# Performance work log

Measured on AMD Instinct MI355X. Metric: run time of the kernel, lower is better.

## Reference

```python
import jax, jax.numpy as jnp
import numpy as np

N_HEADS = 16
N_KV_HEADS = 4
N_EMBD = 1024

def setup_inputs() -> dict:
    key = jax.random.key(0)
    kx, kq, kk, kv, ko = jax.random.split(key, 5)
    B, S, E = 2, 2048, N_EMBD
    head_dim = E // N_HEADS
    kv_dim = N_KV_HEADS * head_dim  # 256
    scale = 0.02
    return {
        "x": jax.random.normal(kx, (B, S, E), dtype=jnp.float32),
        "Wq": jax.random.normal(kq, (E, E), dtype=jnp.float32) * scale,
        "Wk": jax.random.normal(kk, (E, kv_dim), dtype=jnp.float32) * scale,
        "Wv": jax.random.normal(kv, (E, kv_dim), dtype=jnp.float32) * scale,
        "Wo": jax.random.normal(ko, (E, E), dtype=jnp.float32) * scale,
    }

def reference(x, Wq, Wk, Wv, Wo):
    B, S, E = x.shape
    H, KV = N_HEADS, N_KV_HEADS
    D = E // H            # head_dim = 64
    R = H // KV           # query heads per kv head = 4
    inv_sqrt_d = 1.0 / (D ** 0.5)

    q = (x @ Wq).reshape(B, S, KV, R, D)   # group query heads by kv group
    k = (x @ Wk).reshape(B, S, KV, D)
    v = (x @ Wv).reshape(B, S, KV, D)

    # repeat_interleave(kv, R, dim=heads) == broadcast kv head g to query heads (g, r)
    scores = jnp.einsum('bqgrd,bkgd->bgrqk', q, k) * inv_sqrt_d  # [B,KV,R,S,S]
    causal = jnp.tril(jnp.ones((S, S), dtype=bool))
    scores = jnp.where(causal, scores, jnp.float32(-jnp.inf))
    attn = jax.nn.softmax(scores, axis=-1)

    out = jnp.einsum('bgrqk,bkgd->bqgrd', attn, v).reshape(B, S, E)
    return out @ Wo
```

## Files before the change

kernel.cpp:

```cpp
#include <hip/hip_runtime.h>
#include <hip/hip_bf16.h>

#define B_SZ   2
#define S_LEN  2048
#define E_DIM  1024
#define H_Q    16
#define H_KV   4
#define HD     64
#define KV_DIM 256
#define M_ROWS (B_SZ * S_LEN)
#define N_QT   (S_LEN / 64)

typedef short bf16x4 __attribute__((ext_vector_type(4)));
typedef short bf16x8 __attribute__((ext_vector_type(8)));
typedef float f32x4  __attribute__((ext_vector_type(4)));
typedef unsigned u32x2 __attribute__((ext_vector_type(2)));

#define MFMA16x32(a, b, c) __builtin_amdgcn_mfma_f32_16x16x32_bf16(a, b, c, 0, 0, 0)

#if __has_builtin(__builtin_amdgcn_mfma_f32_16x16x16bf16_1k)
#define MFMA_PV(a, b, c) __builtin_amdgcn_mfma_f32_16x16x16bf16_1k(a, b, c, 0, 0, 0)
#elif __has_builtin(__builtin_amdgcn_mfma_f32_16x16x16_bf16)
#define MFMA_PV(a, b, c) __builtin_amdgcn_mfma_f32_16x16x16_bf16(a, b, c, 0, 0, 0)
#else
static __device__ inline f32x4 mfma_pv_asm(bf16x4 a, bf16x4 b, f32x4 c) {
    asm volatile("v_mfma_f32_16x16x16_bf16 %0, %1, %2, %0"
                 : "+v"(c) : "v"(a), "v"(b));
    return c;
}
#define MFMA_PV(a, b, c) mfma_pv_asm(a, b, c)
#endif

static __device__ __forceinline__ short f32_to_bf16(float f) {
    unsigned u = __builtin_bit_cast(unsigned, f);
    u += 0x7fffu + ((u >> 16) & 1u);
    return (short)(u >> 16);
}

static __device__ __forceinline__ unsigned pack2_trunc(float a, float b) {
    unsigned ua = __builtin_bit_cast(unsigned, a);
    unsigned ub = __builtin_bit_cast(unsigned, b);
    return (ua >> 16) | (ub & 0xffff0000u);
}

static __device__ __forceinline__ void load_lds16(const short* g, short* l) {
    __builtin_amdgcn_global_load_lds(
        (const __attribute__((address_space(1))) void*)g,
        (__attribute__((address_space(3))) void*)l, 16, 0, 0);
}

__device__ __forceinline__ void transpose_body(const float* __restrict__ W,
                                               short* __restrict__ Wt,
                                               int K, int N, int bx, int by) {
    __shared__ float t[32][33];
    const int n0 = bx * 32, k0 = by * 32;
    const int tx = threadIdx.x & 31, ty = threadIdx.x >> 5;
#pragma unroll
    for (int i = 0; i < 32; i += 8)
        t[ty + i][tx] = W[(long)(k0 + ty + i) * N + n0 + tx];
    __syncthreads();
#pragma unroll
    for (int i = 0; i < 32; i += 8)
        Wt[(long)(n0 + ty + i) * K + k0 + tx] = f32_to_bf16(t[tx][ty + i]);
}

__global__ __launch_bounds__(256)
void prep(const float* __restrict__ x,
          const float* __restrict__ Wq, const float* __restrict__ Wk,
          const float* __restrict__ Wv, const float* __restrict__ Wo,
          short* __restrict__ xbf, short* __restrict__ Wqt,
          short* __restrict__ Wkt, short* __restrict__ Wvt,
          short* __restrict__ Wot) {
    const int bid = blockIdx.x;
    if (bid < 4096) {
        const int i = bid * 256 + threadIdx.x;
        float4 v = ((const float4*)x)[i];
        bf16x4 o;
        o[0] = f32_to_bf16(v.x); o[1] = f32_to_bf16(v.y);
        o[2] = f32_to_bf16(v.z); o[3] = f32_to_bf16(v.w);
        ((bf16x4*)xbf)[i] = o;
    } else if (bid < 5120) {
        const int r = bid - 4096;
        transpose_body(Wq, Wqt, E_DIM, E_DIM, r & 31, r >> 5);
    } else if (bid < 5376) {
        const int r = bid - 5120;
        transpose_body(Wk, Wkt, E_DIM, KV_DIM, r & 7, r >> 3);
    } else if (bid < 5632) {
        const int r = bid - 5376;
        transpose_body(Wv, Wvt, E_DIM, KV_DIM, r & 7, r >> 3);
    } else {
        const int r = bid - 5632;
        transpose_body(Wo, Wot, E_DIM, E_DIM, r & 31, r >> 5);
    }
}

__global__ __launch_bounds__(256)
void transpose_v(const short* __restrict__ V, short* __restrict__ Vt) {
    const int st = blockIdx.x;
    const int gb = blockIdx.y;
    const int g  = gb >> 1, b = gb & 1;
    const int s0 = st * 64;
    __shared__ short Ls[64][72];
#pragma unroll
    for (int it = 0; it < 2; ++it) {
        const int slot = threadIdx.x + it * 256;
        const int si = slot >> 3, ch = slot & 7;
        *(bf16x8*)&Ls[si][ch * 8] = *(const bf16x8*)
            &V[((long)(b * S_LEN + s0 + si)) * KV_DIM + g * HD + ch * 8];
    }
    __syncthreads();
#pragma unroll
    for (int it = 0; it < 2; ++it) {
        const int slot = threadIdx.x + it * 256;
        const int d = slot >> 3, ch = slot & 7;
        bf16x8 v;
#pragma unroll
        for (int i = 0; i < 8; ++i) v[i] = Ls[ch * 8 + i][d];
        *(bf16x8*)&Vt[((long)(gb * HD + d)) * S_LEN + s0 + ch * 8] = v;
    }
}

__device__ __forceinline__ void gemm128(const short* __restrict__ Ab,
                                        const short* __restrict__ Btb,
                                        int K, short* As, short* Bs,
                                        f32x4 acc[4][4]) {
    const int tid  = threadIdx.x;
    const int wave = tid >> 6;
    const int lane = tid & 63;
    const int lq   = lane & 15;
    const int lg   = lane >> 4;
    const int wm   = wave >> 1;
    const int wn   = wave & 1;
    const int lrow = lane >> 2;
    const int lkc  = (lane & 3) * 8;

#pragma unroll
    for (int i = 0; i < 4; ++i)
#pragma unroll
        for (int j = 0; j < 4; ++j) acc[i][j] = (f32x4){0.f, 0.f, 0.f, 0.f};

    for (int k0 = 0; k0 < K; k0 += 32) {
        __syncthreads();
#pragma unroll
        for (int it = 0; it < 2; ++it) {
            const int m0 = wave * 32 + it * 16;
            const int m  = m0 + lrow;
            load_lds16(Ab  + (size_t)m * K + k0 + lkc, As + m0 * 32);
            load_lds16(Btb + (size_t)m * K + k0 + lkc, Bs + m0 * 32);
        }
        __syncthreads();
        bf16x8 af[4], bfr[4];
#pragma unroll
        for (int i = 0; i < 4; ++i) {
            af[i]  = *(const bf16x8*)&As[(wm * 64 + i * 16 + lq) * 32 + lg * 8];
            bfr[i] = *(const bf16x8*)&Bs[(wn * 64 + i * 16 + lq) * 32 + lg * 8];
        }
#pragma unroll
        for (int i = 0; i < 4; ++i)
#pragma unroll
            for (int j = 0; j < 4; ++j)
                acc[i][j] = MFMA16x32(af[i], bfr[j], acc[i][j]);
    }
}

__global__ __launch_bounds__(256)
void qkv_gemm(const short* __restrict__ xbf,
              const short* __restrict__ Wqt, const short* __restrict__ Wkt,
              const short* __restrict__ Wvt,
              short* __restrict__ Qbf, short* __restrict__ Kbf,
              short* __restrict__ Vbf, float qscale) {
    __shared__ short As[128 * 32];
    __shared__ short Bs[128 * 32];
    const int nb = blockIdx.x;
    const int mb = blockIdx.y;
    const short* Bt; short* out; int ldc, ncol0; float alpha;
    if (nb < 8) {
        Bt = Wqt + (size_t)nb * 128 * E_DIM;
        out = Qbf; ldc = E_DIM; ncol0 = nb * 128; alpha = qscale;
    } else if (nb < 10) {
        Bt = Wkt + (size_t)(nb - 8) * 128 * E_DIM;
        out = Kbf; ldc = KV_DIM; ncol0 = (nb - 8) * 128; alpha = 1.f;
    } else {
        Bt = Wvt + (size_t)(nb - 10) * 128 * E_DIM;
        out = Vbf; ldc = KV_DIM; ncol0 = (nb - 10) * 128; alpha = 1.f;
    }
    f32x4 acc[4][4];
    gemm128(xbf + (size_t)mb * 128 * E_DIM, Bt, E_DIM, As, Bs, acc);

    const int lane = threadIdx.x & 63, wave = threadIdx.x >> 6;
    const int lq = lane & 15, lg = lane >> 4, wm = wave >> 1, wn = wave & 1;
#pragma unroll
    for (int i = 0; i < 4; ++i)
#pragma unroll
        for (int r = 0; r < 4; ++r) {
            const size_t row = (size_t)mb * 128 + wm * 64 + i * 16 + lg * 4 + r;
#pragma unroll
            for (int j = 0; j < 4; ++j)
                out[row * ldc + ncol0 + wn * 64 + j * 16 + lq] =
                    f32_to_bf16(acc[i][j][r] * alpha);
        }
}

__global__ __launch_bounds__(256)
void gemm_o(const short* __restrict__ Abf, const short* __restrict__ Wot,
            float* __restrict__ C) {
    __shared__ short As[128 * 32];
    __shared__ short Bs[128 * 32];
    const int nb = blockIdx.x;
    const int mb = blockIdx.y;
    f32x4 acc[4][4];
    gemm128(Abf + (size_t)mb * 128 * E_DIM,
            Wot + (size_t)nb * 128 * E_DIM, E_DIM, As, Bs, acc);

    const int lane = threadIdx.x & 63, wave = threadIdx.x >> 6;
    const int lq = lane & 15, lg = lane >> 4, wm = wave >> 1, wn = wave & 1;
#pragma unroll
    for (int i = 0; i < 4; ++i)
#pragma unroll
        for (int r = 0; r < 4; ++r) {
            const size_t row = (size_t)mb * 128 + wm * 64 + i * 16 + lg * 4 + r;
#pragma unroll
            for (int j = 0; j < 4; ++j)
                C[row * E_DIM + nb * 128 + wn * 64 + j * 16 + lq] =
                    acc[i][j][r];
        }
}

struct KVregs { bf16x8 k[2], v[2]; };

__device__ __forceinline__ void stage_load(const short* __restrict__ Kb,
                                           const short* __restrict__ Vtg,
                                           long b, long ks, int g,
                                           KVregs& kv) {
    const int tid = threadIdx.x;
#pragma unroll
    for (int it = 0; it < 2; ++it) {
        const int c   = tid + it * 256;
        const int row = c >> 3;
        const int ch  = c & 7;
        kv.k[it] = *(const bf16x8*)
            &Kb[(b * S_LEN + ks + row) * KV_DIM + g * HD + ch * 8];
        kv.v[it] = *(const bf16x8*)
            &Vtg[((long)(g * 2 + b) * HD + row) * S_LEN + ks + ch * 8];
    }
}

__device__ __forceinline__ void stage_write(short (*Ks)[72], short (*Vt)[72],
                                            const KVregs& kv) {
    const int tid = threadIdx.x;
#pragma unroll
    for (int it = 0; it < 2; ++it) {
        const int c   = tid + it * 256;
        const int row = c >> 3;
        const int ch  = c & 7;
        *(bf16x8*)&Ks[row][ch * 8] = kv.k[it];
        *(bf16x8*)&Vt[row][ch * 8] = kv.v[it];
    }
}

__global__ __launch_bounds__(256)
void flash_mfma(const short* __restrict__ Qb,
                const short* __restrict__ Kb,
                const short* __restrict__ Vtg,
                short* __restrict__ Ob) {
    const int pair = blockIdx.x;
    const int h    = blockIdx.y;
    const int b    = blockIdx.z;
    const int g    = h >> 2;

    const int tid  = threadIdx.x;
    const int wave = tid >> 6;
    const int lane = tid & 63;
    const int lq   = lane & 15;
    const int lg   = lane >> 4;

    __shared__ short Ks[2][64][72];
    __shared__ short Vt[2][64][72];

    for (int rep = 0; rep < 2; ++rep) {
        const int qt = rep ? (N_QT - 1 - pair) : pair;
        const int qs = qt * 64;

        const short* qrow =
            Qb + ((long)(b * S_LEN + qs + wave * 16 + lq)) * E_DIM + h * HD;
        const bf16x8 qf0 = *(const bf16x8*)(qrow + lg * 8);
        const bf16x8 qf1 = *(const bf16x8*)(qrow + 32 + lg * 8);

        f32x4 o[4];
#pragma unroll
        for (int dc = 0; dc < 4; ++dc) o[dc] = (f32x4){0.f, 0.f, 0.f, 0.f};
        float l_run = 0.f;

        KVregs kv;
        stage_load(Kb, Vtg, b, 0, g, kv);
        stage_write(Ks[0], Vt[0], kv);
        __syncthreads();

        int p = 0;
        for (int kt = 0; kt <= qt; ++kt) {
            if (kt < qt)
                stage_load(Kb, Vtg, b, (long)(kt + 1) * 64, g, kv);

            const int cmax = (kt == qt) ? wave : 3;
            f32x4 s[4];
#pragma unroll
            for (int c = 0; c < 4; ++c) {
                if (c > cmax) continue;
                bf16x8 kf0 = *(const bf16x8*)&Ks[p][c * 16 + lq][lg * 8];
                bf16x8 kf1 = *(const bf16x8*)&Ks[p][c * 16 + lq][32 + lg * 8];
                f32x4 acc = (f32x4){0.f, 0.f, 0.f, 0.f};
                acc = MFMA16x32(kf0, qf0, acc);
                acc = MFMA16x32(kf1, qf1, acc);
                s[c] = acc;
            }

            if (kt == qt) {
#pragma unroll
                for (int r = 0; r < 4; ++r)
                    if (lg * 4 + r > lq) s[wave][r] = -INFINITY;
            }

            float psum = 0.f;
#pragma unroll
            for (int c = 0; c < 4; ++c) {
                if (c > cmax) continue;
#pragma unroll
                for (int r = 0; r < 4; ++r) {
                    float pe = exp2f(s[c][r]);
                    s[c][r] = pe;
                    psum += pe;
                }
            }
            l_run += psum;

#pragma unroll
            for (int c = 0; c < 4; ++c) {
                if (c > cmax) continue;
                u32x2 packed;
                packed[0] = pack2_trunc(s[c][0], s[c][1]);
                packed[1] = pack2_trunc(s[c][2], s[c][3]);
                bf16x4 pa = __builtin_bit_cast(bf16x4, packed);
#pragma unroll
                for (int dc = 0; dc < 4; ++dc) {
                    bf16x4 vf =
                        *(const bf16x4*)&Vt[p][dc * 16 + lq][c * 16 + lg * 4];
                    o[dc] = MFMA_PV(pa, vf, o[dc]);
                }
            }

            if (kt < qt) stage_write(Ks[p ^ 1], Vt[p ^ 1], kv);
            __syncthreads();
            p ^= 1;
        }

        l_run += __shfl_xor(l_run, 16);
        l_run += __shfl_xor(l_run, 32);

#pragma unroll
        for (int r = 0; r < 4; ++r) {
            const float lT  = __shfl(l_run, lg * 4 + r);
            const float inv = 1.f / lT;
            const long base =
                ((long)(b * S_LEN + qs + wave * 16 + lg * 4 + r)) * E_DIM +
                h * HD + lq;
#pragma unroll
            for (int dc = 0; dc < 4; ++dc)
                Ob[base + dc * 16] = f32_to_bf16(o[dc][r] * inv);
        }
    }
}

extern "C" void kernel_launch(void* const* d_in, const int* in_sizes, int n_in,
                              void* d_out, int out_size, void* d_ws, size_t ws_size,
                              hipStream_t stream) {
    const float* x  = (const float*)d_in[0];
    const float* Wq = (const float*)d_in[1];
    const float* Wk = (const float*)d_in[2];
    const float* Wv = (const float*)d_in[3];
    const float* Wo = (const float*)d_in[4];
    float* out = (float*)d_out;

    short* xbf = (short*)d_ws;
    short* Wqt = xbf + (size_t)M_ROWS * E_DIM;
    short* Wkt = Wqt + (size_t)E_DIM * E_DIM;
    short* Wvt = Wkt + (size_t)KV_DIM * E_DIM;
    short* Wot = Wvt + (size_t)KV_DIM * E_DIM;
    short* Qbf = Wot + (size_t)E_DIM * E_DIM;
    short* Kbf = Qbf + (size_t)M_ROWS * E_DIM;
    short* Vbf = Kbf + (size_t)M_ROWS * KV_DIM;
    short* Abf = Vbf + (size_t)M_ROWS * KV_DIM;
    short* Vtg = Abf + (size_t)M_ROWS * E_DIM;

    const float qscale = 0.125f * 1.44269504088896340736f;

    prep<<<dim3(6656), dim3(256), 0, stream>>>(
        x, Wq, Wk, Wv, Wo, xbf, Wqt, Wkt, Wvt, Wot);
    qkv_gemm<<<dim3(12, M_ROWS / 128), dim3(256), 0, stream>>>(
        xbf, Wqt, Wkt, Wvt, Qbf, Kbf, Vbf, qscale);
    transpose_v<<<dim3(S_LEN / 64, B_SZ * H_KV), dim3(256), 0, stream>>>(
        Vbf, Vtg);
    flash_mfma<<<dim3(N_QT / 2, H_Q, B_SZ), dim3(256), 0, stream>>>(
        Qbf, Kbf, Vtg, Abf);
    gemm_o<<<dim3(E_DIM / 128, M_ROWS / 128), dim3(256), 0, stream>>>(
        Abf, Wot, out);
}
```

Baseline: 181.6 us.

## Split flash attention over KV halves with merge kernel; fuse V transpose into QKV GEMM

```diff
diff --git a/kernel.cpp b/kernel.cpp
--- a/kernel.cpp
+++ b/kernel.cpp
@@ -94,32 +94,6 @@
     }
 }
 
-__global__ __launch_bounds__(256)
-void transpose_v(const short* __restrict__ V, short* __restrict__ Vt) {
-    const int st = blockIdx.x;
-    const int gb = blockIdx.y;
-    const int g  = gb >> 1, b = gb & 1;
-    const int s0 = st * 64;
-    __shared__ short Ls[64][72];
-#pragma unroll
-    for (int it = 0; it < 2; ++it) {
-        const int slot = threadIdx.x + it * 256;
-        const int si = slot >> 3, ch = slot & 7;
-        *(bf16x8*)&Ls[si][ch * 8] = *(const bf16x8*)
-            &V[((long)(b * S_LEN + s0 + si)) * KV_DIM + g * HD + ch * 8];
-    }
-    __syncthreads();
-#pragma unroll
-    for (int it = 0; it < 2; ++it) {
-        const int slot = threadIdx.x + it * 256;
-        const int d = slot >> 3, ch = slot & 7;
-        bf16x8 v;
-#pragma unroll
-        for (int i = 0; i < 8; ++i) v[i] = Ls[ch * 8 + i][d];
-        *(bf16x8*)&Vt[((long)(gb * HD + d)) * S_LEN + s0 + ch * 8] = v;
-    }
-}
-
 __device__ __forceinline__ void gemm128(const short* __restrict__ Ab,
                                         const short* __restrict__ Btb,
                                         int K, short* As, short* Bs,
@@ -168,37 +142,54 @@
               const short* __restrict__ Wqt, const short* __restrict__ Wkt,
               const short* __restrict__ Wvt,
               short* __restrict__ Qbf, short* __restrict__ Kbf,
-              short* __restrict__ Vbf, float qscale) {
+              short* __restrict__ Vtg, float qscale) {
     __shared__ short As[128 * 32];
     __shared__ short Bs[128 * 32];
     const int nb = blockIdx.x;
     const int mb = blockIdx.y;
-    const short* Bt; short* out; int ldc, ncol0; float alpha;
-    if (nb < 8) {
-        Bt = Wqt + (size_t)nb * 128 * E_DIM;
-        out = Qbf; ldc = E_DIM; ncol0 = nb * 128; alpha = qscale;
-    } else if (nb < 10) {
-        Bt = Wkt + (size_t)(nb - 8) * 128 * E_DIM;
-        out = Kbf; ldc = KV_DIM; ncol0 = (nb - 8) * 128; alpha = 1.f;
-    } else {
-        Bt = Wvt + (size_t)(nb - 10) * 128 * E_DIM;
-        out = Vbf; ldc = KV_DIM; ncol0 = (nb - 10) * 128; alpha = 1.f;
-    }
+    const short* Bt;
+    if (nb < 8)       Bt = Wqt + (size_t)nb * 128 * E_DIM;
+    else if (nb < 10) Bt = Wkt + (size_t)(nb - 8) * 128 * E_DIM;
+    else              Bt = Wvt + (size_t)(nb - 10) * 128 * E_DIM;
+
     f32x4 acc[4][4];
     gemm128(xbf + (size_t)mb * 128 * E_DIM, Bt, E_DIM, As, Bs, acc);
 
     const int lane = threadIdx.x & 63, wave = threadIdx.x >> 6;
     const int lq = lane & 15, lg = lane >> 4, wm = wave >> 1, wn = wave & 1;
-#pragma unroll
-    for (int i = 0; i < 4; ++i)
-#pragma unroll
-        for (int r = 0; r < 4; ++r) {
-            const size_t row = (size_t)mb * 128 + wm * 64 + i * 16 + lg * 4 + r;
-#pragma unroll
-            for (int j = 0; j < 4; ++j)
-                out[row * ldc + ncol0 + wn * 64 + j * 16 + lq] =
-                    f32_to_bf16(acc[i][j][r] * alpha);
-        }
+
+    if (nb < 10) {
+        short* out; int ldc, ncol0; float alpha;
+        if (nb < 8) { out = Qbf; ldc = E_DIM; ncol0 = nb * 128; alpha = qscale; }
+        else { out = Kbf; ldc = KV_DIM; ncol0 = (nb - 8) * 128; alpha = 1.f; }
+#pragma unroll
+        for (int i = 0; i < 4; ++i)
+#pragma unroll
+            for (int r = 0; r < 4; ++r) {
+                const size_t row =
+                    (size_t)mb * 128 + wm * 64 + i * 16 + lg * 4 + r;
+#pragma unroll
+                for (int j = 0; j < 4; ++j)
+                    out[row * ldc + ncol0 + wn * 64 + j * 16 + lq] =
+                        f32_to_bf16(acc[i][j][r] * alpha);
+            }
+    } else {
+        const int ncol0 = (nb - 10) * 128;
+#pragma unroll
+        for (int i = 0; i < 4; ++i)
+#pragma unroll
+            for (int r = 0; r < 4; ++r) {
+                const int row = mb * 128 + wm * 64 + i * 16 + lg * 4 + r;
+                const int bb = row >> 11, s = row & 2047;
+#pragma unroll
+                for (int j = 0; j < 4; ++j) {
+                    const int col = ncol0 + wn * 64 + j * 16 + lq;
+                    const int gg = col >> 6, d = col & 63;
+                    Vtg[((long)(gg * 2 + bb) * HD + d) * S_LEN + s] =
+                        f32_to_bf16(acc[i][j][r]);
+                }
+            }
+    }
 }
 
 __global__ __launch_bounds__(256)
@@ -262,11 +253,13 @@
 void flash_mfma(const short* __restrict__ Qb,
                 const short* __restrict__ Kb,
                 const short* __restrict__ Vtg,
-                short* __restrict__ Ob) {
-    const int pair = blockIdx.x;
-    const int h    = blockIdx.y;
-    const int b    = blockIdx.z;
-    const int g    = h >> 2;
+                float* __restrict__ Op,
+                float* __restrict__ Lp) {
+    const int pair  = blockIdx.x;
+    const int h     = blockIdx.y;
+    const int b     = blockIdx.z >> 1;
+    const int split = blockIdx.z & 1;
+    const int g     = h >> 2;
 
     const int tid  = threadIdx.x;
     const int wave = tid >> 6;
@@ -280,6 +273,9 @@
     for (int rep = 0; rep < 2; ++rep) {
         const int qt = rep ? (N_QT - 1 - pair) : pair;
         const int qs = qt * 64;
+        const int half = (qt + 1) >> 1;
+        const int kt0  = split ? half : 0;
+        const int kt1  = split ? qt : half - 1;
 
         const short* qrow =
             Qb + ((long)(b * S_LEN + qs + wave * 16 + lq)) * E_DIM + h * HD;
@@ -291,83 +287,108 @@
         for (int dc = 0; dc < 4; ++dc) o[dc] = (f32x4){0.f, 0.f, 0.f, 0.f};
         float l_run = 0.f;
 
-        KVregs kv;
-        stage_load(Kb, Vtg, b, 0, g, kv);
-        stage_write(Ks[0], Vt[0], kv);
-        __syncthreads();
-
-        int p = 0;
-        for (int kt = 0; kt <= qt; ++kt) {
-            if (kt < qt)
-                stage_load(Kb, Vtg, b, (long)(kt + 1) * 64, g, kv);
-
-            const int cmax = (kt == qt) ? wave : 3;
-            f32x4 s[4];
-#pragma unroll
-            for (int c = 0; c < 4; ++c) {
-                if (c > cmax) continue;
-                bf16x8 kf0 = *(const bf16x8*)&Ks[p][c * 16 + lq][lg * 8];
-                bf16x8 kf1 = *(const bf16x8*)&Ks[p][c * 16 + lq][32 + lg * 8];
-                f32x4 acc = (f32x4){0.f, 0.f, 0.f, 0.f};
-                acc = MFMA16x32(kf0, qf0, acc);
-                acc = MFMA16x32(kf1, qf1, acc);
-                s[c] = acc;
+        if (kt0 <= kt1) {
+            KVregs kv;
+            stage_load(Kb, Vtg, b, (long)kt0 * 64, g, kv);
+            stage_write(Ks[0], Vt[0], kv);
+            __syncthreads();
+
+            int p = 0;
+            for (int kt = kt0; kt <= kt1; ++kt) {
+                if (kt < kt1)
+                    stage_load(Kb, Vtg, b, (long)(kt + 1) * 64, g, kv);
+
+                const int cmax = (kt == qt) ? wave : 3;
+                f32x4 s[4];
+#pragma unroll
+                for (int c = 0; c < 4; ++c) {
+                    if (c > cmax) continue;
+                    bf16x8 kf0 = *(const bf16x8*)&Ks[p][c * 16 + lq][lg * 8];
+                    bf16x8 kf1 =
+                        *(const bf16x8*)&Ks[p][c * 16 + lq][32 + lg * 8];
+                    f32x4 acc = (f32x4){0.f, 0.f, 0.f, 0.f};
+                    acc = MFMA16x32(kf0, qf0, acc);
+                    acc = MFMA16x32(kf1, qf1, acc);
+                    s[c] = acc;
+                }
+
+                if (kt == qt) {
+#pragma unroll
+                    for (int r = 0; r < 4; ++r)
+                        if (lg * 4 + r > lq) s[wave][r] = -INFINITY;
+                }
+
+                float psum = 0.f;
+#pragma unroll
+                for (int c = 0; c < 4; ++c) {
+                    if (c > cmax) continue;
+#pragma unroll
+                    for (int r = 0; r < 4; ++r) {
+                        float pe = exp2f(s[c][r]);
+                        s[c][r] = pe;
+                        psum += pe;
+                    }
+                }
+                l_run += psum;
+
+#pragma unroll
+                for (int c = 0; c < 4; ++c) {
+                    if (c > cmax) continue;
+                    u32x2 packed;
+                    packed[0] = pack2_trunc(s[c][0], s[c][1]);
+                    packed[1] = pack2_trunc(s[c][2], s[c][3]);
+                    bf16x4 pa = __builtin_bit_cast(bf16x4, packed);
+#pragma unroll
+                    for (int dc = 0; dc < 4; ++dc) {
+                        bf16x4 vf = *(const bf16x4*)
+                            &Vt[p][dc * 16 + lq][c * 16 + lg * 4];
+                        o[dc] = MFMA_PV(pa, vf, o[dc]);
+                    }
+                }
+
+                if (kt < kt1) stage_write(Ks[p ^ 1], Vt[p ^ 1], kv);
+                __syncthreads();
+                p ^= 1;
             }
-
-            if (kt == qt) {
-#pragma unroll
-                for (int r = 0; r < 4; ++r)
-                    if (lg * 4 + r > lq) s[wave][r] = -INFINITY;
-            }
-
-            float psum = 0.f;
-#pragma unroll
-            for (int c = 0; c < 4; ++c) {
-                if (c > cmax) continue;
-#pragma unroll
-                for (int r = 0; r < 4; ++r) {
-                    float pe = exp2f(s[c][r]);
-                    s[c][r] = pe;
-                    psum += pe;
-                }
-            }
-            l_run += psum;
-
-#pragma unroll
-            for (int c = 0; c < 4; ++c) {
-                if (c > cmax) continue;
-                u32x2 packed;
-                packed[0] = pack2_trunc(s[c][0], s[c][1]);
-                packed[1] = pack2_trunc(s[c][2], s[c][3]);
-                bf16x4 pa = __builtin_bit_cast(bf16x4, packed);
-#pragma unroll
-                for (int dc = 0; dc < 4; ++dc) {
-                    bf16x4 vf =
-                        *(const bf16x4*)&Vt[p][dc * 16 + lq][c * 16 + lg * 4];
-                    o[dc] = MFMA_PV(pa, vf, o[dc]);
-                }
-            }
-
-            if (kt < qt) stage_write(Ks[p ^ 1], Vt[p ^ 1], kv);
-            __syncthreads();
-            p ^= 1;
         }
 
         l_run += __shfl_xor(l_run, 16);
         l_run += __shfl_xor(l_run, 32);
 
+        const long ibase = (long)(split * 2 + b) << 21;
 #pragma unroll
         for (int r = 0; r < 4; ++r) {
-            const float lT  = __shfl(l_run, lg * 4 + r);
-            const float inv = 1.f / lT;
-            const long base =
-                ((long)(b * S_LEN + qs + wave * 16 + lg * 4 + r)) * E_DIM +
-                h * HD + lq;
-#pragma unroll
-            for (int dc = 0; dc < 4; ++dc)
-                Ob[base + dc * 16] = f32_to_bf16(o[dc][r] * inv);
+            const long base = ibase +
+                ((long)(qs + wave * 16 + lg * 4 + r)) * E_DIM + h * HD + lq;
+#pragma unroll
+            for (int dc = 0; dc < 4; ++dc) Op[base + dc * 16] = o[dc][r];
         }
-    }
+        if (lg == 0)
+            Lp[((split * 2 + b) * H_Q + h) * S_LEN + qs + wave * 16 + lq] =
+                l_run;
+    }
+}
+
+__global__ __launch_bounds__(256)
+void merge_o(const float* __restrict__ Op, const float* __restrict__ Lp,
+             short* __restrict__ Abf) {
+    const long idx4 = (long)blockIdx.x * 256 + threadIdx.x;
+    const long e = idx4 * 4;
+    const int b  = (int)(e >> 21);
+    const long ei = e & ((1L << 21) - 1);
+    const int s  = (int)(ei >> 10);
+    const int hh = ((int)(ei & 1023)) >> 6;
+    const float4 v0 = *(const float4*)(Op + ((long)(0 + b) << 21) + ei);
+    const float4 v1 = *(const float4*)(Op + ((long)(2 + b) << 21) + ei);
+    const float l = Lp[((0 + b) * H_Q + hh) * S_LEN + s] +
+                    Lp[((2 + b) * H_Q + hh) * S_LEN + s];
+    const float inv = 1.f / l;
+    bf16x4 o;
+    o[0] = f32_to_bf16((v0.x + v1.x) * inv);
+    o[1] = f32_to_bf16((v0.y + v1.y) * inv);
+    o[2] = f32_to_bf16((v0.z + v1.z) * inv);
+    o[3] = f32_to_bf16((v0.w + v1.w) * inv);
+    *(bf16x4*)(Abf + e) = o;
 }
 
 extern "C" void kernel_launch(void* const* d_in, const int* in_sizes, int n_in,
@@ -387,20 +408,21 @@
     short* Wot = Wvt + (size_t)KV_DIM * E_DIM;
     short* Qbf = Wot + (size_t)E_DIM * E_DIM;
     short* Kbf = Qbf + (size_t)M_ROWS * E_DIM;
-    short* Vbf = Kbf + (size_t)M_ROWS * KV_DIM;
-    short* Abf = Vbf + (size_t)M_ROWS * KV_DIM;
-    short* Vtg = Abf + (size_t)M_ROWS * E_DIM;
+    short* Vtg = Kbf + (size_t)M_ROWS * KV_DIM;
+    short* Abf = Vtg + (size_t)8 * HD * S_LEN;
+    float* Op  = (float*)(Abf + (size_t)M_ROWS * E_DIM);
+    float* Lp  = Op + (size_t)4 * S_LEN * E_DIM;
 
     const float qscale = 0.125f * 1.44269504088896340736f;
 
     prep<<<dim3(6656), dim3(256), 0, stream>>>(
         x, Wq, Wk, Wv, Wo, xbf, Wqt, Wkt, Wvt, Wot);
     qkv_gemm<<<dim3(12, M_ROWS / 128), dim3(256), 0, stream>>>(
-        xbf, Wqt, Wkt, Wvt, Qbf, Kbf, Vbf, qscale);
-    transpose_v<<<dim3(S_LEN / 64, B_SZ * H_KV), dim3(256), 0, stream>>>(
-        Vbf, Vtg);
-    flash_mfma<<<dim3(N_QT / 2, H_Q, B_SZ), dim3(256), 0, stream>>>(
-        Qbf, Kbf, Vtg, Abf);
+        xbf, Wqt, Wkt, Wvt, Qbf, Kbf, Vtg, qscale);
+    flash_mfma<<<dim3(N_QT / 2, H_Q, 4), dim3(256), 0, stream>>>(
+        Qbf, Kbf, Vtg, Op, Lp);
+    merge_o<<<dim3(M_ROWS * E_DIM / 4 / 256), dim3(256), 0, stream>>>(
+        Op, Lp, Abf);
     gemm_o<<<dim3(E_DIM / 128, M_ROWS / 128), dim3(256), 0, stream>>>(
         Abf, Wot, out);
 }
```

Result: slower. 198.3 us (+9.1%).
